# Performance work log

Measured on AMD Instinct MI355X. Metric: run time of the kernel, lower is better.

Reference implementation:

```python
import jax, jax.numpy as jnp
import numpy as np

WD, WH, WW = 2, 7, 7
N = WD * WH * WW          # 98 tokens per window
DIM = 128
HEADS = 4
HEAD_DIM = DIM // HEADS   # 32
B_ = 2048                 # num_windows * batch
NW = 64                   # windows per image (mask leading dim)
TABLE = (2 * WD - 1) * (2 * WH - 1) * (2 * WW - 1)  # 507


def _relative_position_index():
    coords = np.stack(np.meshgrid(np.arange(WD), np.arange(WH), np.arange(WW), indexing='ij'))
    flat = coords.reshape(3, -1)                     # [3, N]
    rel = flat[:, :, None] - flat[:, None, :]        # [3, N, N]
    rel = rel.transpose(1, 2, 0).copy()              # [N, N, 3]
    rel[:, :, 0] += WD - 1
    rel[:, :, 1] += WH - 1
    rel[:, :, 2] += WW - 1
    rel[:, :, 0] *= (2 * WH - 1) * (2 * WW - 1)
    rel[:, :, 1] *= 2 * WW - 1
    return rel.sum(-1).astype(np.int32)             # [N, N]


def setup_inputs() -> dict:
    key = jax.random.key(0)
    ks = jax.random.split(key, 6)
    x = jax.random.normal(ks[0], (B_, N, DIM), dtype=jnp.float32)
    mask = jax.random.normal(ks[1], (NW, N, N), dtype=jnp.float32)
    qkv_w = jax.random.normal(ks[2], (3 * DIM, DIM), dtype=jnp.float32) * 0.02
    qkv_b = jnp.zeros((3 * DIM,), dtype=jnp.float32)
    proj_w = jax.random.normal(ks[3], (DIM, DIM), dtype=jnp.float32) * 0.02
    proj_b = jnp.zeros((DIM,), dtype=jnp.float32)
    bias_table = jax.random.normal(ks[4], (TABLE, HEADS), dtype=jnp.float32) * 0.02
    rel_idx = jnp.asarray(_relative_position_index())
    return {"x": x, "mask": mask, "qkv_w": qkv_w, "qkv_b": qkv_b,
            "proj_w": proj_w, "proj_b": proj_b, "bias_table": bias_table,
            "rel_idx": rel_idx}


def reference(x, mask, qkv_w, qkv_b, proj_w, proj_b, bias_table, rel_idx):
    b, n, c = x.shape
    hd = c // HEADS
    scale = hd ** -0.5
    qkv = x @ qkv_w.T + qkv_b                          # [B_, N, 3C]
    qkv = qkv.reshape(b, n, 3, HEADS, hd)
    qkv = jnp.transpose(qkv, (2, 0, 3, 1, 4))          # [3, B_, H, N, hd]
    q, k, v = qkv[0], qkv[1], qkv[2]
    attn = jnp.einsum('bhnd,bhmd->bhnm', q * scale, k)  # [B_, H, N, N]
    # gathered relative position bias
    bias = bias_table[rel_idx.reshape(-1)].reshape(n, n, HEADS)
    bias = jnp.transpose(bias, (2, 0, 1))               # [H, N, N]
    attn = attn + bias[None]
    nw = mask.shape[0]
    attn = attn.reshape(b // nw, nw, HEADS, n, n) + mask[None, :, None]
    attn = jax.nn.softmax(attn.reshape(b, HEADS, n, n), axis=-1)
    out = jnp.einsum('bhnm,bhmd->bnhd', attn, v).reshape(b, n, c)
    out = out @ proj_w.T + proj_b
    return out
```

## Files before the change

### kernel.cpp

```cpp
#include <hip/hip_runtime.h>
#include <stdint.h>

#define NTOK 98
#define DIM 128
#define HEADS 4
#define HD 32
#define BWIN 2048
#define NW 64
#define SCALE 0.17677669529663687f
#define QSTR 32
#define VSTR 104

typedef __bf16 bf16_t;
typedef bf16_t bf16x8 __attribute__((ext_vector_type(8)));
typedef float f32x4 __attribute__((ext_vector_type(4)));
typedef unsigned short u16;
typedef unsigned int u32;
typedef unsigned long long u64;

__device__ __forceinline__ u16 f2bf(float f) {
    union { bf16_t h; u16 u; } v; v.h = (bf16_t)f; return v.u;
}
__device__ __forceinline__ float bf2f(u16 b) {
    union { u16 u; bf16_t h; } v; v.u = b; return (float)v.h;
}
__device__ __forceinline__ int qk_idx(int row, int d) {
    return row * QSTR + ((((d >> 3) ^ (row & 3)) << 3) | (d & 7));
}

__global__ void k0_prep(const float* __restrict__ qkv_w, const float* __restrict__ proj_w,
                        const float* __restrict__ mask,
                        const float* __restrict__ bias_table, const int* __restrict__ rel_idx,
                        const float* __restrict__ x,
                        u16* __restrict__ qkvw_bf, u16* __restrict__ pw_bf,
                        u16* __restrict__ mbT, u16* __restrict__ xbf)
{
    int t = blockIdx.x * 256 + threadIdx.x;
    if (t < 49152) {
        qkvw_bf[t] = f2bf(qkv_w[t]);
    } else if (t < 65536) {
        int r = t - 49152;
        pw_bf[r] = f2bf(proj_w[r]);
    } else if (t < 3276800) {
        int r = t - 65536;
        int w    = r / 50176;
        int rem  = r - w * 50176;
        int hh   = rem / 12544;
        int rem2 = rem - hh * 12544;
        int i    = rem2 >> 7;
        int c    = rem2 & 127;
        int l16  = c >> 3;
        int njp  = c & 7;
        int j    = njp * 16 + l16;
        float val = -1e30f;
        if (njp < 7 && j < NTOK)
            val = mask[w * 9604 + i * NTOK + j] + bias_table[rel_idx[i * NTOK + j] * HEADS + hh];
        mbT[r] = f2bf(val);
    } else if (t < 6488064) {
        size_t idx = (size_t)(t - 3276800) * 8;
        const float4 a0 = *reinterpret_cast<const float4*>(x + idx);
        const float4 a1 = *reinterpret_cast<const float4*>(x + idx + 4);
        u64 p0 = (u64)f2bf(a0.x) | ((u64)f2bf(a0.y) << 16) |
                 ((u64)f2bf(a0.z) << 32) | ((u64)f2bf(a0.w) << 48);
        u64 p1 = (u64)f2bf(a1.x) | ((u64)f2bf(a1.y) << 16) |
                 ((u64)f2bf(a1.z) << 32) | ((u64)f2bf(a1.w) << 48);
        *reinterpret_cast<u64*>(&xbf[idx])     = p0;
        *reinterpret_cast<u64*>(&xbf[idx + 4]) = p1;
    }
}

__global__ __launch_bounds__(256, 5) void k_attn(
    const u16* __restrict__ xbf, const u16* __restrict__ qkvw_bf,
    const float* __restrict__ qkv_b, const u16* __restrict__ mbT,
    u16* __restrict__ OG)
{
    __shared__ __align__(16) u16 qL[NTOK * QSTR];
    __shared__ __align__(16) u16 kL[NTOK * QSTR];
    __shared__ __align__(16) u16 vL[HD * VSTR];
    __shared__ __align__(16) u16 Pscr[4][16 * VSTR];

    const int bh   = (blockIdx.x & 7) * 1024 + (blockIdx.x >> 3);
    const int b    = bh >> 2;
    const int h    = bh & 3;
    const int tid  = threadIdx.x;
    const int wave = tid >> 6;
    const int lane = tid & 63;
    const int l16  = lane & 15;
    const int quad = lane >> 4;

    const u16* xb = xbf + (size_t)b * (NTOK * DIM);

    {
        const int u0 = (wave * 21) >> 2;
        const int u1 = ((wave + 1) * 21) >> 2;
        int cached = -1;
        bf16x8 Bf[2][4];
        float  cb[2];
        for (int u = u0; u < u1; ++u) {
            const int part = u / 7;
            const int mt   = u - part * 7;
            if (part != cached) {
                const u16* wp = qkvw_bf + (size_t)part * DIM * DIM;
#pragma unroll
                for (int nt2 = 0; nt2 < 2; ++nt2) {
                    const int col = h * HD + nt2 * 16 + l16;
#pragma unroll
                    for (int ks = 0; ks < 4; ++ks)
                        Bf[nt2][ks] = *reinterpret_cast<const bf16x8*>(
                            wp + col * DIM + quad * 8 + ks * 32);
                    cb[nt2] = qkv_b[part * DIM + col];
                }
                cached = part;
            }
            int arow = mt * 16 + l16;
            if (arow > 97) arow = 97;
            bf16x8 af[4];
#pragma unroll
            for (int ks = 0; ks < 4; ++ks)
                af[ks] = *reinterpret_cast<const bf16x8*>(
                    xb + arow * DIM + quad * 8 + ks * 32);
            f32x4 acc0 = {0.f, 0.f, 0.f, 0.f};
            f32x4 acc1 = {0.f, 0.f, 0.f, 0.f};
            __builtin_amdgcn_s_setprio(1);
#pragma unroll
            for (int ks = 0; ks < 4; ++ks) {
                acc0 = __builtin_amdgcn_mfma_f32_16x16x32_bf16(af[ks], Bf[0][ks], acc0, 0, 0, 0);
                acc1 = __builtin_amdgcn_mfma_f32_16x16x32_bf16(af[ks], Bf[1][ks], acc1, 0, 0, 0);
            }
            __builtin_amdgcn_s_setprio(0);
            const int tokb = mt * 16 + quad * 4;
#pragma unroll
            for (int nt2 = 0; nt2 < 2; ++nt2) {
                const f32x4& acc = nt2 ? acc1 : acc0;
                const int d = nt2 * 16 + l16;
                const float cbv = cb[nt2];
                if (part == 0) {
#pragma unroll
                    for (int reg = 0; reg < 4; ++reg) {
                        int tok = tokb + reg;
                        if (tok < NTOK)
                            qL[qk_idx(tok, d)] = f2bf((acc[reg] + cbv) * SCALE);
                    }
                } else if (part == 1) {
#pragma unroll
                    for (int reg = 0; reg < 4; ++reg) {
                        int tok = tokb + reg;
                        if (tok < NTOK)
                            kL[qk_idx(tok, d)] = f2bf(acc[reg] + cbv);
                    }
                } else {
                    u16* vrow = &vL[d * VSTR];
                    if (tokb + 3 <= 97) {
                        u64 pack = 0;
#pragma unroll
                        for (int reg = 0; reg < 4; ++reg)
                            pack |= ((u64)f2bf(acc[reg] + cbv)) << (16 * reg);
                        *reinterpret_cast<u64*>(&vrow[tokb]) = pack;
                    } else if (tokb <= 97) {
                        u32 pack = (u32)f2bf(acc[0] + cbv) | ((u32)f2bf(acc[1] + cbv) << 16);
                        *reinterpret_cast<u32*>(&vrow[tokb]) = pack;
                    }
                }
            }
        }
    }
    __syncthreads();

    {
        const u16* mbtp = mbT + ((size_t)((b & (NW - 1)) * HEADS + h)) * (NTOK * 128);
        u16* ps = &Pscr[wave][0];
        const int qko = ((quad ^ (l16 & 3)) << 3);

        bf16x8 kf[7];
#pragma unroll
        for (int nj = 0; nj < 7; ++nj) {
            int krow = nj * 16 + l16;
            if (krow > 97) krow = 97;
            kf[nj] = *reinterpret_cast<const bf16x8*>(&kL[krow * QSTR + qko]);
        }

        for (int mi = 0; mi < 2; ++mi) {
            const int mt = wave + mi * 4;
            if (mt > 6) break;
            bf16x8 mrows[4];
#pragma unroll
            for (int reg = 0; reg < 4; ++reg) {
                int i  = mt * 16 + quad * 4 + reg;
                int ic = (i > 97) ? 97 : i;
                mrows[reg] = *reinterpret_cast<const bf16x8*>(&mbtp[ic * 128 + l16 * 8]);
            }
            int qrow = mt * 16 + l16;
            if (qrow > 97) qrow = 97;
            bf16x8 qf = *reinterpret_cast<const bf16x8*>(&qL[qrow * QSTR + qko]);
            f32x4 sacc[7];
            __builtin_amdgcn_s_setprio(1);
#pragma unroll
            for (int nj = 0; nj < 7; ++nj) {
                f32x4 z = {0.f, 0.f, 0.f, 0.f};
                sacc[nj] = __builtin_amdgcn_mfma_f32_16x16x32_bf16(qf, kf[nj], z, 0, 0, 0);
            }
            __builtin_amdgcn_s_setprio(0);
            float rin[4];
#pragma unroll
            for (int reg = 0; reg < 4; ++reg) {
                float s[7];
#pragma unroll
                for (int nj = 0; nj < 7; ++nj)
                    s[nj] = sacc[nj][reg] + (float)mrows[reg][nj];
                float mx = fmaxf(fmaxf(fmaxf(s[0], s[1]), fmaxf(s[2], s[3])),
                                 fmaxf(fmaxf(s[4], s[5]), s[6]));
#pragma unroll
                for (int off = 1; off < 16; off <<= 1) mx = fmaxf(mx, __shfl_xor(mx, off));
                float p[7];
                float lsum = 0.f;
#pragma unroll
                for (int nj = 0; nj < 7; ++nj) {
                    p[nj] = __expf(s[nj] - mx);
                    lsum += p[nj];
                }
                u16* psr = &ps[(quad * 4 + reg) * VSTR];
#pragma unroll
                for (int nj = 0; nj < 6; ++nj)
                    psr[nj * 16 + l16] = f2bf(p[nj]);
                if (l16 < 8) psr[96 + l16] = f2bf(p[6]);
#pragma unroll
                for (int off = 1; off < 16; off <<= 1) lsum += __shfl_xor(lsum, off);
                rin[reg] = 1.f / lsum;
            }
            bf16x8 pf[3];
#pragma unroll
            for (int ks = 0; ks < 3; ++ks)
                pf[ks] = *reinterpret_cast<const bf16x8*>(&ps[l16 * VSTR + quad * 8 + ks * 32]);
#pragma unroll
            for (int nt = 0; nt < 2; ++nt) {
                f32x4 oacc = {0.f, 0.f, 0.f, 0.f};
                __builtin_amdgcn_s_setprio(1);
#pragma unroll
                for (int ks = 0; ks < 3; ++ks) {
                    bf16x8 vf = *reinterpret_cast<const bf16x8*>(
                        &vL[(nt * 16 + l16) * VSTR + quad * 8 + ks * 32]);
                    oacc = __builtin_amdgcn_mfma_f32_16x16x32_bf16(pf[ks], vf, oacc, 0, 0, 0);
                }
                __builtin_amdgcn_s_setprio(0);
                int d = nt * 16 + l16;
                float v96 = bf2f(vL[d * VSTR + 96]);
                float v97 = bf2f(vL[d * VSTR + 97]);
#pragma unroll
                for (int reg = 0; reg < 4; ++reg) {
                    int i = mt * 16 + quad * 4 + reg;
                    if (i < NTOK) {
                        float p96 = bf2f(ps[(quad * 4 + reg) * VSTR + 96]);
                        float p97 = bf2f(ps[(quad * 4 + reg) * VSTR + 97]);
                        OG[((size_t)b * NTOK + i) * DIM + h * HD + d] =
                            f2bf((oacc[reg] + p96 * v96 + p97 * v97) * rin[reg]);
                    }
                }
            }
        }
    }
}

__global__ __launch_bounds__(256, 4) void k_proj(
    const u16* __restrict__ OG, const u16* __restrict__ pw_bf,
    const float* __restrict__ proj_b, float* __restrict__ out)
{
    const int b    = ((blockIdx.x & 7) << 8) + (blockIdx.x >> 3);
    const int tid  = threadIdx.x;
    const int wave = tid >> 6;
    const int lane = tid & 63;
    const int l16  = lane & 15;
    const int quad = lane >> 4;

    bf16x8 bw[2][4];
    float  pb[2];
#pragma unroll
    for (int nt2 = 0; nt2 < 2; ++nt2) {
        const int col = (wave * 2 + nt2) * 16 + l16;
#pragma unroll
        for (int ks = 0; ks < 4; ++ks)
            bw[nt2][ks] = *reinterpret_cast<const bf16x8*>(
                pw_bf + col * DIM + quad * 8 + ks * 32);
        pb[nt2] = proj_b[col];
    }
    const u16* ob = OG + (size_t)b * (NTOK * DIM);
    for (int mt = 0; mt < 7; ++mt) {
        int arow = mt * 16 + l16;
        if (arow > 97) arow = 97;
        bf16x8 af[4];
#pragma unroll
        for (int ks = 0; ks < 4; ++ks)
            af[ks] = *reinterpret_cast<const bf16x8*>(ob + arow * DIM + quad * 8 + ks * 32);
        f32x4 acc0 = {0.f, 0.f, 0.f, 0.f};
        f32x4 acc1 = {0.f, 0.f, 0.f, 0.f};
#pragma unroll
        for (int ks = 0; ks < 4; ++ks) {
            acc0 = __builtin_amdgcn_mfma_f32_16x16x32_bf16(af[ks], bw[0][ks], acc0, 0, 0, 0);
            acc1 = __builtin_amdgcn_mfma_f32_16x16x32_bf16(af[ks], bw[1][ks], acc1, 0, 0, 0);
        }
#pragma unroll
        for (int nt2 = 0; nt2 < 2; ++nt2) {
            const f32x4& acc = nt2 ? acc1 : acc0;
            const int col = (wave * 2 + nt2) * 16 + l16;
#pragma unroll
            for (int reg = 0; reg < 4; ++reg) {
                int row = mt * 16 + quad * 4 + reg;
                if (row < NTOK)
                    out[((size_t)b * NTOK + row) * DIM + col] = acc[reg] + pb[nt2];
            }
        }
    }
}

extern "C" void kernel_launch(void* const* d_in, const int* in_sizes, int n_in,
                              void* d_out, int out_size, void* d_ws, size_t ws_size,
                              hipStream_t stream)
{
    const float* x       = (const float*)d_in[0];
    const float* mask    = (const float*)d_in[1];
    const float* qkv_w   = (const float*)d_in[2];
    const float* qkv_b   = (const float*)d_in[3];
    const float* proj_w  = (const float*)d_in[4];
    const float* proj_b  = (const float*)d_in[5];
    const float* bias_tb = (const float*)d_in[6];
    const int*   rel_idx = (const int*)d_in[7];
    float* out = (float*)d_out;

    char* ws = (char*)d_ws;
    u16* qkvw_bf = (u16*)(ws + 0);
    u16* pw_bf   = (u16*)(ws + 98304);
    u16* mbT     = (u16*)(ws + 131072);
    u16* xbf     = (u16*)(ws + 6553600);
    u16* OG      = (u16*)(ws + 57933824);

    k0_prep<<<25344, 256, 0, stream>>>(qkv_w, proj_w, mask, bias_tb, rel_idx, x,
                                       qkvw_bf, pw_bf, mbT, xbf);
    k_attn<<<BWIN * HEADS, 256, 0, stream>>>(xbf, qkvw_bf, qkv_b, mbT, OG);
    k_proj<<<BWIN, 256, 0, stream>>>(OG, pw_bf, proj_b, out);
}
```

Measured before the change: 367.2 us.

## Interleave second tile's QK MFMA with first softmax and stage proj A in LDS

The attention kernel now computes the first row tile's scores and softmax, then issues the second tile's QK MFMAs and mask loads before the first tile's PV, so matrix work can overlap softmax and PV of the other tile. The projection kernel stages each window's 98x128 attention output in padded shared memory instead of having all four waves re-read it from global memory, and raises its occupancy hint. This costs more live registers in the attention kernel and extra LDS per block in the projection kernel.

Measured after the change: 356.1 us. 1.03x faster.

```diff
diff --git a/kernel.cpp b/kernel.cpp
--- a/kernel.cpp
+++ b/kernel.cpp
@@ -179,28 +179,7 @@
             kf[nj] = *reinterpret_cast<const bf16x8*>(&kL[krow * QSTR + qko]);
         }
 
-        for (int mi = 0; mi < 2; ++mi) {
-            const int mt = wave + mi * 4;
-            if (mt > 6) break;
-            bf16x8 mrows[4];
-#pragma unroll
-            for (int reg = 0; reg < 4; ++reg) {
-                int i  = mt * 16 + quad * 4 + reg;
-                int ic = (i > 97) ? 97 : i;
-                mrows[reg] = *reinterpret_cast<const bf16x8*>(&mbtp[ic * 128 + l16 * 8]);
-            }
-            int qrow = mt * 16 + l16;
-            if (qrow > 97) qrow = 97;
-            bf16x8 qf = *reinterpret_cast<const bf16x8*>(&qL[qrow * QSTR + qko]);
-            f32x4 sacc[7];
-            __builtin_amdgcn_s_setprio(1);
-#pragma unroll
-            for (int nj = 0; nj < 7; ++nj) {
-                f32x4 z = {0.f, 0.f, 0.f, 0.f};
-                sacc[nj] = __builtin_amdgcn_mfma_f32_16x16x32_bf16(qf, kf[nj], z, 0, 0, 0);
-            }
-            __builtin_amdgcn_s_setprio(0);
-            float rin[4];
+        auto softmax_tile = [&](const f32x4* sacc, const bf16x8* mrows, float* rin) {
 #pragma unroll
             for (int reg = 0; reg < 4; ++reg) {
                 float s[7];
@@ -227,6 +206,9 @@
                 for (int off = 1; off < 16; off <<= 1) lsum += __shfl_xor(lsum, off);
                 rin[reg] = 1.f / lsum;
             }
+        };
+
+        auto pv_store = [&](int mt, const float* rin) {
             bf16x8 pf[3];
 #pragma unroll
             for (int ks = 0; ks < 3; ++ks)
@@ -256,14 +238,67 @@
                     }
                 }
             }
-        }
-    }
-}
-
-__global__ __launch_bounds__(256, 4) void k_proj(
+        };
+
+        const int mt1 = wave;
+        const int mt2 = wave + 4;
+        const bool has2 = (mt2 < 7);
+
+        bf16x8 mrows1[4];
+#pragma unroll
+        for (int reg = 0; reg < 4; ++reg) {
+            int i = mt1 * 16 + quad * 4 + reg;
+            mrows1[reg] = *reinterpret_cast<const bf16x8*>(&mbtp[i * 128 + l16 * 8]);
+        }
+        bf16x8 qf1 = *reinterpret_cast<const bf16x8*>(&qL[(mt1 * 16 + l16) * QSTR + qko]);
+        f32x4 sacc1[7];
+        __builtin_amdgcn_s_setprio(1);
+#pragma unroll
+        for (int nj = 0; nj < 7; ++nj) {
+            f32x4 z = {0.f, 0.f, 0.f, 0.f};
+            sacc1[nj] = __builtin_amdgcn_mfma_f32_16x16x32_bf16(qf1, kf[nj], z, 0, 0, 0);
+        }
+        __builtin_amdgcn_s_setprio(0);
+
+        float rin1[4];
+        softmax_tile(sacc1, mrows1, rin1);
+
+        f32x4 sacc2[7];
+        bf16x8 mrows2[4];
+        if (has2) {
+            int qrow2 = mt2 * 16 + l16;
+            if (qrow2 > 97) qrow2 = 97;
+            bf16x8 qf2 = *reinterpret_cast<const bf16x8*>(&qL[qrow2 * QSTR + qko]);
+            __builtin_amdgcn_s_setprio(1);
+#pragma unroll
+            for (int nj = 0; nj < 7; ++nj) {
+                f32x4 z = {0.f, 0.f, 0.f, 0.f};
+                sacc2[nj] = __builtin_amdgcn_mfma_f32_16x16x32_bf16(qf2, kf[nj], z, 0, 0, 0);
+            }
+            __builtin_amdgcn_s_setprio(0);
+#pragma unroll
+            for (int reg = 0; reg < 4; ++reg) {
+                int i  = mt2 * 16 + quad * 4 + reg;
+                int ic = (i > 97) ? 97 : i;
+                mrows2[reg] = *reinterpret_cast<const bf16x8*>(&mbtp[ic * 128 + l16 * 8]);
+            }
+        }
+
+        pv_store(mt1, rin1);
+        if (has2) {
+            float rin2[4];
+            softmax_tile(sacc2, mrows2, rin2);
+            pv_store(mt2, rin2);
+        }
+    }
+}
+
+__global__ __launch_bounds__(256, 6) void k_proj(
     const u16* __restrict__ OG, const u16* __restrict__ pw_bf,
     const float* __restrict__ proj_b, float* __restrict__ out)
 {
+    __shared__ __align__(16) u16 A[98 * 136];
+
     const int b    = ((blockIdx.x & 7) << 8) + (blockIdx.x >> 3);
     const int tid  = threadIdx.x;
     const int wave = tid >> 6;
@@ -282,14 +317,23 @@
                 pw_bf + col * DIM + quad * 8 + ks * 32);
         pb[nt2] = proj_b[col];
     }
+
     const u16* ob = OG + (size_t)b * (NTOK * DIM);
+    for (int idx = tid; idx < (NTOK * DIM / 8); idx += 256) {
+        int row = idx >> 4;
+        int c8  = idx & 15;
+        *reinterpret_cast<bf16x8*>(&A[row * 136 + c8 * 8]) =
+            *reinterpret_cast<const bf16x8*>(ob + row * DIM + c8 * 8);
+    }
+    __syncthreads();
+
     for (int mt = 0; mt < 7; ++mt) {
         int arow = mt * 16 + l16;
         if (arow > 97) arow = 97;
         bf16x8 af[4];
 #pragma unroll
         for (int ks = 0; ks < 4; ++ks)
-            af[ks] = *reinterpret_cast<const bf16x8*>(ob + arow * DIM + quad * 8 + ks * 32);
+            af[ks] = *reinterpret_cast<const bf16x8*>(&A[arow * 136 + quad * 8 + ks * 32]);
         f32x4 acc0 = {0.f, 0.f, 0.f, 0.f};
         f32x4 acc1 = {0.f, 0.f, 0.f, 0.f};
 #pragma unroll
```
